# Performance work log

Measured on AMD Instinct MI355X. Metric: run time of the kernel, lower is better.

Reference implementation:

```python
import jax, jax.numpy as jnp
import numpy as np

N_NODES = 50000


def gat_layer(x, src, dst, W, att_s, att_d, b, concat):
    # PyG GATConv (eval mode): h = x W reshaped to [N, H, C]
    H, C = att_s.shape
    h = (x @ W).reshape(-1, H, C)                      # [N, H, C]
    a_s = (h * att_s).sum(-1)                          # [N, H]
    a_d = (h * att_d).sum(-1)                          # [N, H]
    e = jax.nn.leaky_relu(a_s[src] + a_d[dst], 0.2)    # [E, H]
    # scatter-softmax over destination nodes
    m = jax.ops.segment_max(e, dst, num_segments=N_NODES)
    alpha = jnp.exp(e - m[dst])
    denom = jax.ops.segment_sum(alpha, dst, num_segments=N_NODES)
    alpha = alpha / denom[dst]                         # [E, H]
    msg = h[src] * alpha[:, :, None]                   # [E, H, C]
    out = jax.ops.segment_sum(msg, dst, num_segments=N_NODES)  # [N, H, C]
    out = out.reshape(N_NODES, H * C) if concat else out.mean(axis=1)
    return out + b


def setup_inputs() -> dict:
    key = jax.random.key(0)
    ks = jax.random.split(key, 16)
    F_IN, HID, HEADS, NCLS, E = 512, 64, 4, 40, 800000
    x = jax.random.normal(ks[0], (N_NODES, F_IN), dtype=jnp.float32)
    edge_index = jax.random.randint(ks[1], (2, E), 0, N_NODES, dtype=jnp.int32)

    def glorot(k, shape):
        fan = shape[0]
        return jax.random.normal(k, shape, dtype=jnp.float32) / np.sqrt(fan)

    d1 = HID * HEADS  # 256
    return {
        "x": x,
        "edge_index": edge_index,
        "W1": glorot(ks[2], (F_IN, d1)),
        "as1": glorot(ks[3], (HEADS, HID)),
        "ad1": glorot(ks[4], (HEADS, HID)),
        "b1": jnp.zeros((d1,), jnp.float32),
        "W2": glorot(ks[5], (d1, d1)),
        "as2": glorot(ks[6], (HEADS, HID)),
        "ad2": glorot(ks[7], (HEADS, HID)),
        "b2": jnp.zeros((d1,), jnp.float32),
        "W3": glorot(ks[8], (d1, NCLS)),
        "as3": glorot(ks[9], (1, NCLS)),
        "ad3": glorot(ks[10], (1, NCLS)),
        "b3": jnp.zeros((NCLS,), jnp.float32),
    }


def reference(x, edge_index, W1, as1, ad1, b1, W2, as2, ad2, b2, W3, as3, ad3, b3):
    # add self-loops (PyG GATConv default)
    loops = jnp.arange(N_NODES, dtype=edge_index.dtype)
    src = jnp.concatenate([edge_index[0], loops])
    dst = jnp.concatenate([edge_index[1], loops])
    h = jax.nn.elu(gat_layer(x, src, dst, W1, as1, ad1, b1, True))
    h = jax.nn.elu(gat_layer(h, src, dst, W2, as2, ad2, b2, True))
    out = gat_layer(h, src, dst, W3, as3, ad3, b3, False)
    return out
```

## Files before the change

### kernel.cpp

```cpp
#include <hip/hip_runtime.h>
#include <stdint.h>

#define NN 50000
#define NB 196

typedef unsigned short u16;
typedef _Float16 f16;
typedef __attribute__((ext_vector_type(8))) _Float16 half8;
typedef __attribute__((ext_vector_type(4))) _Float16 half4;
typedef __attribute__((ext_vector_type(4))) float f32x4;


__global__ void count_k(const int* __restrict__ dst, int* __restrict__ cnt, int E){
  int i = blockIdx.x * 256 + threadIdx.x;
  int tot = E + NN;
  if (i >= tot) return;
  int d = (i < E) ? dst[i] : (i - E);
  atomicAdd(&cnt[d], 1);
}

__global__ __launch_bounds__(256) void scan_part_k(const int* __restrict__ cnt,
                                                   int* __restrict__ bsum){
  __shared__ int lds[256];
  int tid = threadIdx.x;
  int idx = blockIdx.x * 256 + tid;
  lds[tid] = (idx < NN) ? cnt[idx] : 0;
  __syncthreads();
#pragma unroll
  for (int off = 128; off >= 1; off >>= 1){
    if (tid < off) lds[tid] += lds[tid + off];
    __syncthreads();
  }
  if (tid == 0) bsum[blockIdx.x] = lds[0];
}

__global__ __launch_bounds__(256) void scan_top_k(const int* __restrict__ bsum,
                                                  int* __restrict__ boff,
                                                  int* __restrict__ row_ptr){
  __shared__ int lds[256];
  int tid = threadIdx.x;
  int v = (tid < NB) ? bsum[tid] : 0;
  lds[tid] = v;
  __syncthreads();
#pragma unroll
  for (int off = 1; off < 256; off <<= 1){
    int t = (tid >= off) ? lds[tid - off] : 0;
    __syncthreads();
    lds[tid] += t;
    __syncthreads();
  }
  if (tid < NB) boff[tid] = lds[tid] - v;
  if (tid == 255) row_ptr[NN] = lds[255];
}

__global__ __launch_bounds__(256) void scan_fin_k(const int* __restrict__ cnt,
                                                  const int* __restrict__ boff,
                                                  int* __restrict__ row_ptr,
                                                  int* __restrict__ cursor){
  __shared__ int lds[256];
  int tid = threadIdx.x;
  int idx = blockIdx.x * 256 + tid;
  int v = (idx < NN) ? cnt[idx] : 0;
  lds[tid] = v;
  __syncthreads();
#pragma unroll
  for (int off = 1; off < 256; off <<= 1){
    int t = (tid >= off) ? lds[tid - off] : 0;
    __syncthreads();
    lds[tid] += t;
    __syncthreads();
  }
  if (idx < NN){
    int r = boff[blockIdx.x] + lds[tid] - v;
    row_ptr[idx] = r;
    cursor[idx]  = r;
  }
}

__global__ void scatter_k(const int* __restrict__ src, const int* __restrict__ dst,
                          int* __restrict__ cursor, int* __restrict__ csr, int E){
  int i = blockIdx.x * 256 + threadIdx.x;
  int tot = E + NN;
  if (i >= tot) return;
  int s, d;
  if (i < E){ s = src[i]; d = dst[i]; } else { s = i - E; d = i - E; }
  int pos = atomicAdd(&cursor[d], 1);
  csr[pos] = s;
}


__global__ void transpose_k(const float* __restrict__ W, f16* __restrict__ Wt, int K, int N){
  int i = blockIdx.x * 256 + threadIdx.x;
  if (i >= K * N) return;
  int n = i / K, k = i - n * K;
  Wt[i] = (f16)W[k * N + n];
}


template<bool A_FP32>
__global__ __launch_bounds__(256) void gemm_wide_k(const void* __restrict__ Aptr,
                                                   const f16* __restrict__ Bt,
                                                   f16* __restrict__ C,
                                                   int M, int K){
  __shared__ f16 As[64 * 40];
  __shared__ f16 Bs[256 * 40];
  const int tid  = threadIdx.x;
  const int wave = tid >> 6, lane = tid & 63;
  const int quad = lane >> 4, l16 = lane & 15;
  const int m0 = blockIdx.x * 64;
  const int srow = tid >> 2;
  const int scol = (tid & 3) * 8;

  f32x4 acc[16] = {};

  for (int k0 = 0; k0 < K; k0 += 32){
    half8 va = {0,0,0,0,0,0,0,0};
    int gm = m0 + srow;
    if (gm < M){
      if (A_FP32){
        const float* A = (const float*)Aptr;
        const f32x4 f0 = *(const f32x4*)(A + (size_t)gm * K + k0 + scol);
        const f32x4 f1 = *(const f32x4*)(A + (size_t)gm * K + k0 + scol + 4);
        va[0] = (f16)f0.x; va[1] = (f16)f0.y; va[2] = (f16)f0.z; va[3] = (f16)f0.w;
        va[4] = (f16)f1.x; va[5] = (f16)f1.y; va[6] = (f16)f1.z; va[7] = (f16)f1.w;
      } else {
        va = *(const half8*)((const f16*)Aptr + (size_t)gm * K + k0 + scol);
      }
    }
    *(half8*)(&As[srow * 40 + scol]) = va;

#pragma unroll
    for (int rep = 0; rep < 4; rep++){
      int row = srow + 64 * rep;
      half8 vb = *(const half8*)(Bt + (size_t)row * K + k0 + scol);
      *(half8*)(&Bs[row * 40 + scol]) = vb;
    }

    __syncthreads();
    half8 af = *(const half8*)(&As[(wave * 16 + l16) * 40 + quad * 8]);
#pragma unroll
    for (int i = 0; i < 16; i++){
      half8 bf = *(const half8*)(&Bs[(i * 16 + l16) * 40 + quad * 8]);
      acc[i] = __builtin_amdgcn_mfma_f32_16x16x32_f16(af, bf, acc[i], 0, 0, 0);
    }
    __syncthreads();
  }

#pragma unroll
  for (int i = 0; i < 16; i++){
    int n = i * 16 + l16;
#pragma unroll
    for (int r = 0; r < 4; r++){
      int mm = m0 + wave * 16 + quad * 4 + r;
      if (mm < M) C[(size_t)mm * 256 + n] = (f16)acc[i][r];
    }
  }
}


__global__ __launch_bounds__(256) void gemm_k(const f16* __restrict__ A,
                                              const f16* __restrict__ Bt,
                                              f16* __restrict__ C,
                                              int M, int N, int K){
  __shared__ f16 As[64 * 40];
  __shared__ f16 Bs[64 * 40];
  const int tid  = threadIdx.x;
  const int wave = tid >> 6, lane = tid & 63;
  const int quad = lane >> 4, l16 = lane & 15;
  const int m0 = blockIdx.x * 64, n0 = blockIdx.y * 64;
  const int srow = tid >> 2;
  const int scol = (tid & 3) * 8;

  f32x4 acc[4] = {};

  for (int k0 = 0; k0 < K; k0 += 32){
    half8 va = {0,0,0,0,0,0,0,0};
    int gm = m0 + srow;
    if (gm < M) va = *(const half8*)(A + (size_t)gm * K + k0 + scol);
    *(half8*)(&As[srow * 40 + scol]) = va;

    half8 vb = {0,0,0,0,0,0,0,0};
    int gn = n0 + srow;
    if (gn < N) vb = *(const half8*)(Bt + (size_t)gn * K + k0 + scol);
    *(half8*)(&Bs[srow * 40 + scol]) = vb;

    __syncthreads();
    half8 af = *(const half8*)(&As[(wave * 16 + l16) * 40 + quad * 8]);
#pragma unroll
    for (int i = 0; i < 4; i++){
      half8 bf = *(const half8*)(&Bs[(i * 16 + l16) * 40 + quad * 8]);
      acc[i] = __builtin_amdgcn_mfma_f32_16x16x32_f16(af, bf, acc[i], 0, 0, 0);
    }
    __syncthreads();
  }

#pragma unroll
  for (int i = 0; i < 4; i++){
    int n = n0 + i * 16 + l16;
#pragma unroll
    for (int r = 0; r < 4; r++){
      int m = m0 + wave * 16 + quad * 4 + r;
      if (m < M && n < N) C[(size_t)m * N + n] = (f16)acc[i][r];
    }
  }
}


__global__ __launch_bounds__(256) void attn4_k(const f16* __restrict__ h,
                                               const float* __restrict__ atts,
                                               const float* __restrict__ attd,
                                               float* __restrict__ a_s,
                                               float* __restrict__ a_d){
  int w = blockIdx.x * 4 + (threadIdx.x >> 6);
  if (w >= NN) return;
  int lane = threadIdx.x & 63;
  const half4 hv = *(const half4*)(h + (size_t)w * 256 + lane * 4);
  const f32x4 sv = *(const f32x4*)(atts + lane * 4);
  const f32x4 dv = *(const f32x4*)(attd + lane * 4);
  float h0 = (float)hv.x, h1 = (float)hv.y, h2 = (float)hv.z, h3 = (float)hv.w;
  float ps = h0 * sv.x + h1 * sv.y + h2 * sv.z + h3 * sv.w;
  float pd = h0 * dv.x + h1 * dv.y + h2 * dv.z + h3 * dv.w;
#pragma unroll
  for (int off = 8; off >= 1; off >>= 1){
    ps += __shfl_xor(ps, off);
    pd += __shfl_xor(pd, off);
  }
  if ((lane & 15) == 0){
    a_s[w * 4 + (lane >> 4)] = ps;
    a_d[w * 4 + (lane >> 4)] = pd;
  }
}

__global__ __launch_bounds__(256) void attn1_k(const f16* __restrict__ h,
                                               const float* __restrict__ atts,
                                               const float* __restrict__ attd,
                                               float* __restrict__ a_s,
                                               float* __restrict__ a_d){
  int w = blockIdx.x * 4 + (threadIdx.x >> 6);
  if (w >= NN) return;
  int lane = threadIdx.x & 63;
  float ps = 0.f, pd = 0.f;
  if (lane < 40){
    float hv = (float)h[(size_t)w * 40 + lane];
    ps = hv * atts[lane];
    pd = hv * attd[lane];
  }
#pragma unroll
  for (int off = 32; off >= 1; off >>= 1){
    ps += __shfl_xor(ps, off);
    pd += __shfl_xor(pd, off);
  }
  if (lane == 0){ a_s[w] = ps; a_d[w] = pd; }
}


__device__ __forceinline__ float lrelu(float e){ return e > 0.f ? e : 0.2f * e; }

__global__ __launch_bounds__(256) void agg4_k(const f16* __restrict__ h,
                                              const float* __restrict__ a_s,
                                              const float* __restrict__ a_d,
                                              const int* __restrict__ row_ptr,
                                              const int* __restrict__ csr,
                                              const float* __restrict__ bias,
                                              f16* __restrict__ out){
  int w = blockIdx.x * 4 + (threadIdx.x >> 6);
  if (w >= NN) return;
  int lane = threadIdx.x & 63;
  int head = lane >> 4;
  float ad = a_d[w * 4 + head];
  int beg = row_ptr[w], end = row_ptr[w + 1];

  float m = -1e30f, denom = 0.f;
  float acc0 = 0.f, acc1 = 0.f, acc2 = 0.f, acc3 = 0.f;

  int s0 = csr[beg];
  int s1 = csr[(beg + 1 < end) ? beg + 1 : beg];
  float e0 = a_s[s0 * 4 + head];
  float e1 = a_s[s1 * 4 + head];
  half4 h0 = *(const half4*)(h + (size_t)s0 * 256 + lane * 4);
  half4 h1 = *(const half4*)(h + (size_t)s1 * 256 + lane * 4);

  for (int j = beg; j < end; j += 2){
    int t0 = (j + 2 < end) ? j + 2 : j;
    int t1 = (j + 3 < end) ? j + 3 : j;
    int sp0 = csr[t0], sp1 = csr[t1];
    float ep0 = a_s[sp0 * 4 + head];
    float ep1 = a_s[sp1 * 4 + head];
    half4 hp0 = *(const half4*)(h + (size_t)sp0 * 256 + lane * 4);
    half4 hp1 = *(const half4*)(h + (size_t)sp1 * 256 + lane * 4);

    float ee0 = lrelu(e0 + ad);
    float ee1 = (j + 1 < end) ? lrelu(e1 + ad) : -1e30f;
    float mn = fmaxf(m, fmaxf(ee0, ee1));
    float cold = __expf(m - mn);
    float al0 = __expf(ee0 - mn);
    float al1 = __expf(ee1 - mn);
    denom = denom * cold + al0 + al1;
    acc0 = acc0 * cold + al0 * (float)h0.x + al1 * (float)h1.x;
    acc1 = acc1 * cold + al0 * (float)h0.y + al1 * (float)h1.y;
    acc2 = acc2 * cold + al0 * (float)h0.z + al1 * (float)h1.z;
    acc3 = acc3 * cold + al0 * (float)h0.w + al1 * (float)h1.w;
    m = mn;
    e0 = ep0; e1 = ep1; h0 = hp0; h1 = hp1;
  }

  float inv = 1.f / fmaxf(denom, 1e-30f);
  float o0 = acc0 * inv + bias[lane * 4 + 0];
  float o1 = acc1 * inv + bias[lane * 4 + 1];
  float o2 = acc2 * inv + bias[lane * 4 + 2];
  float o3 = acc3 * inv + bias[lane * 4 + 3];
  o0 = o0 > 0.f ? o0 : __expf(o0) - 1.f;
  o1 = o1 > 0.f ? o1 : __expf(o1) - 1.f;
  o2 = o2 > 0.f ? o2 : __expf(o2) - 1.f;
  o3 = o3 > 0.f ? o3 : __expf(o3) - 1.f;
  half4 r; r.x = (f16)o0; r.y = (f16)o1; r.z = (f16)o2; r.w = (f16)o3;
  *(half4*)(out + (size_t)w * 256 + lane * 4) = r;
}

__global__ __launch_bounds__(256) void agg1_k(const f16* __restrict__ h,
                                              const float* __restrict__ a_s,
                                              const float* __restrict__ a_d,
                                              const int* __restrict__ row_ptr,
                                              const int* __restrict__ csr,
                                              const float* __restrict__ bias,
                                              float* __restrict__ out){
  int w = blockIdx.x * 4 + (threadIdx.x >> 6);
  if (w >= NN) return;
  int lane = threadIdx.x & 63;
  int cl = (lane < 40) ? lane : 0;
  float ad = a_d[w];
  int beg = row_ptr[w], end = row_ptr[w + 1];

  float m = -1e30f, denom = 0.f, acc = 0.f;

  int s0 = csr[beg];
  int s1 = csr[(beg + 1 < end) ? beg + 1 : beg];
  float e0 = a_s[s0];
  float e1 = a_s[s1];
  float h0 = (float)h[(size_t)s0 * 40 + cl];
  float h1 = (float)h[(size_t)s1 * 40 + cl];

  for (int j = beg; j < end; j += 2){
    int t0 = (j + 2 < end) ? j + 2 : j;
    int t1 = (j + 3 < end) ? j + 3 : j;
    int sp0 = csr[t0], sp1 = csr[t1];
    float ep0 = a_s[sp0];
    float ep1 = a_s[sp1];
    float hp0 = (float)h[(size_t)sp0 * 40 + cl];
    float hp1 = (float)h[(size_t)sp1 * 40 + cl];

    float ee0 = lrelu(e0 + ad);
    float ee1 = (j + 1 < end) ? lrelu(e1 + ad) : -1e30f;
    float mn = fmaxf(m, fmaxf(ee0, ee1));
    float cold = __expf(m - mn);
    float al0 = __expf(ee0 - mn);
    float al1 = __expf(ee1 - mn);
    denom = denom * cold + al0 + al1;
    acc = acc * cold + al0 * h0 + al1 * h1;
    m = mn;
    e0 = ep0; e1 = ep1; h0 = hp0; h1 = hp1;
  }

  if (lane < 40){
    float o = acc / fmaxf(denom, 1e-30f) + bias[lane];
    out[(size_t)w * 40 + lane] = o;
  }
}


extern "C" void kernel_launch(void* const* d_in, const int* in_sizes, int n_in,
                              void* d_out, int out_size, void* d_ws, size_t ws_size,
                              hipStream_t stream){
  const float* x   = (const float*)d_in[0];
  const int*   ei  = (const int*)d_in[1];
  const float* W1  = (const float*)d_in[2];
  const float* as1 = (const float*)d_in[3];
  const float* ad1 = (const float*)d_in[4];
  const float* b1  = (const float*)d_in[5];
  const float* W2  = (const float*)d_in[6];
  const float* as2 = (const float*)d_in[7];
  const float* ad2 = (const float*)d_in[8];
  const float* b2  = (const float*)d_in[9];
  const float* W3  = (const float*)d_in[10];
  const float* as3 = (const float*)d_in[11];
  const float* ad3 = (const float*)d_in[12];
  const float* b3  = (const float*)d_in[13];

  const int E = in_sizes[1] / 2;
  const int ETOT = E + NN;
  const int* src_arr = ei;
  const int* dst_arr = ei + E;

  char* ws = (char*)d_ws;
  size_t off = 0;
  auto alloc = [&](size_t bytes) -> void* {
    void* p = ws + off; off += (bytes + 255) & ~(size_t)255; return p;
  };
  int*   cnt     = (int*)  alloc((size_t)NN * 4);
  int*   row_ptr = (int*)  alloc((size_t)(NN + 1) * 4);
  int*   cursor  = (int*)  alloc((size_t)NN * 4);
  int*   csr     = (int*)  alloc((size_t)ETOT * 4);
  int*   bsum    = (int*)  alloc((size_t)256 * 4);
  int*   boff    = (int*)  alloc((size_t)256 * 4);
  f16*   W1t     = (f16*)  alloc((size_t)512 * 256 * 2);
  f16*   W2t     = (f16*)  alloc((size_t)256 * 256 * 2);
  f16*   W3t     = (f16*)  alloc((size_t)256 * 40 * 2);
  float* a_s     = (float*)alloc((size_t)NN * 4 * 4);
  float* a_d     = (float*)alloc((size_t)NN * 4 * 4);
  f16*   hbuf    = (f16*)  alloc((size_t)NN * 256 * 2);
  f16*   xbuf    = (f16*)  alloc((size_t)NN * 256 * 2);
  (void)ws_size; (void)n_in; (void)out_size;

  hipMemsetAsync(cnt, 0, (size_t)NN * 4, stream);
  int egrid = (ETOT + 255) / 256;
  count_k    <<<egrid, 256, 0, stream>>>(dst_arr, cnt, E);
  scan_part_k<<<NB, 256, 0, stream>>>(cnt, bsum);
  scan_top_k <<<1, 256, 0, stream>>>(bsum, boff, row_ptr);
  scan_fin_k <<<NB, 256, 0, stream>>>(cnt, boff, row_ptr, cursor);
  scatter_k  <<<egrid, 256, 0, stream>>>(src_arr, dst_arr, cursor, csr, E);

  transpose_k<<<(512 * 256 + 255) / 256, 256, 0, stream>>>(W1, W1t, 512, 256);
  transpose_k<<<(256 * 256 + 255) / 256, 256, 0, stream>>>(W2, W2t, 256, 256);
  transpose_k<<<(256 * 40  + 255) / 256, 256, 0, stream>>>(W3, W3t, 256, 40);

  dim3 blk(256);
  dim3 gW((NN + 63) / 64);
  dim3 gC((NN + 63) / 64, 1);
  int nodeblocks = (NN + 3) / 4;

  gemm_wide_k<true> <<<gW, blk, 0, stream>>>(x, W1t, hbuf, NN, 512);
  attn4_k<<<nodeblocks, blk, 0, stream>>>(hbuf, as1, ad1, a_s, a_d);
  agg4_k <<<nodeblocks, blk, 0, stream>>>(hbuf, a_s, a_d, row_ptr, csr, b1, xbuf);

  gemm_wide_k<false><<<gW, blk, 0, stream>>>(xbuf, W2t, hbuf, NN, 256);
  attn4_k<<<nodeblocks, blk, 0, stream>>>(hbuf, as2, ad2, a_s, a_d);
  agg4_k <<<nodeblocks, blk, 0, stream>>>(hbuf, a_s, a_d, row_ptr, csr, b2, xbuf);

  gemm_k<<<gC, blk, 0, stream>>>(xbuf, W3t, hbuf, NN, 40, 256);
  attn1_k<<<nodeblocks, blk, 0, stream>>>(hbuf, as3, ad3, a_s, a_d);
  agg1_k <<<nodeblocks, blk, 0, stream>>>(hbuf, a_s, a_d, row_ptr, csr, b3, (float*)d_out);
}
```

Baseline: 592.0 us.

## Retile wide GEMM to 128x128 blocks with 2x2 wave grid and swizzled LDS

Replaces the 64x256 row-strip GEMM with a 128x128 tile kernel where each of four waves computes a 64x64 sub-tile via 4x4 MFMA accumulators, and the grid now spans two column blocks. LDS is stored in an MFMA-fragment-friendly layout so each lane reads contiguous half8 fragments without padding. This raises per-wave register reuse of A and B fragments and cuts LDS reads per MFMA. In exchange it uses more accumulator registers, which may lower occupancy, and the A tile is loaded twice across the two column blocks.

```diff
diff --git a/kernel.cpp b/kernel.cpp
--- a/kernel.cpp
+++ b/kernel.cpp
@@ -98,61 +98,74 @@
 
 
 template<bool A_FP32>
-__global__ __launch_bounds__(256) void gemm_wide_k(const void* __restrict__ Aptr,
+__global__ __launch_bounds__(256) void gemm_tile_k(const void* __restrict__ Aptr,
                                                    const f16* __restrict__ Bt,
                                                    f16* __restrict__ C,
-                                                   int M, int K){
-  __shared__ f16 As[64 * 40];
-  __shared__ f16 Bs[256 * 40];
+                                                   int M, int N, int K){
+  __shared__ f16 As[128 * 32];
+  __shared__ f16 Bs[128 * 32];
   const int tid  = threadIdx.x;
   const int wave = tid >> 6, lane = tid & 63;
   const int quad = lane >> 4, l16 = lane & 15;
-  const int m0 = blockIdx.x * 64;
+  const int wm = wave >> 1, wn = wave & 1;
+  const int m0 = blockIdx.x * 128, n0 = blockIdx.y * 128;
   const int srow = tid >> 2;
-  const int scol = (tid & 3) * 8;
-
-  f32x4 acc[16] = {};
+  const int sc   = tid & 3;
+
+  f32x4 acc[4][4] = {};
 
   for (int k0 = 0; k0 < K; k0 += 32){
-    half8 va = {0,0,0,0,0,0,0,0};
-    int gm = m0 + srow;
-    if (gm < M){
-      if (A_FP32){
-        const float* A = (const float*)Aptr;
-        const f32x4 f0 = *(const f32x4*)(A + (size_t)gm * K + k0 + scol);
-        const f32x4 f1 = *(const f32x4*)(A + (size_t)gm * K + k0 + scol + 4);
-        va[0] = (f16)f0.x; va[1] = (f16)f0.y; va[2] = (f16)f0.z; va[3] = (f16)f0.w;
-        va[4] = (f16)f1.x; va[5] = (f16)f1.y; va[6] = (f16)f1.z; va[7] = (f16)f1.w;
-      } else {
-        va = *(const half8*)((const f16*)Aptr + (size_t)gm * K + k0 + scol);
+#pragma unroll
+    for (int rep = 0; rep < 2; rep++){
+      int row = rep * 64 + srow;
+      int gm = m0 + row;
+      half8 va = {0,0,0,0,0,0,0,0};
+      if (gm < M){
+        if (A_FP32){
+          const float* A = (const float*)Aptr + (size_t)gm * K + k0 + sc * 8;
+          const f32x4 f0 = *(const f32x4*)(A);
+          const f32x4 f1 = *(const f32x4*)(A + 4);
+          va[0] = (f16)f0.x; va[1] = (f16)f0.y; va[2] = (f16)f0.z; va[3] = (f16)f0.w;
+          va[4] = (f16)f1.x; va[5] = (f16)f1.y; va[6] = (f16)f1.z; va[7] = (f16)f1.w;
+        } else {
+          va = *(const half8*)((const f16*)Aptr + (size_t)gm * K + k0 + sc * 8);
+        }
       }
+      *(half8*)(&As[(((row >> 4) * 64) + sc * 16 + (row & 15)) * 8]) = va;
     }
-    *(half8*)(&As[srow * 40 + scol]) = va;
-
-#pragma unroll
-    for (int rep = 0; rep < 4; rep++){
-      int row = srow + 64 * rep;
-      half8 vb = *(const half8*)(Bt + (size_t)row * K + k0 + scol);
-      *(half8*)(&Bs[row * 40 + scol]) = vb;
+#pragma unroll
+    for (int rep = 0; rep < 2; rep++){
+      int row = rep * 64 + srow;
+      half8 vb = *(const half8*)(Bt + (size_t)(n0 + row) * K + k0 + sc * 8);
+      *(half8*)(&Bs[(((row >> 4) * 64) + sc * 16 + (row & 15)) * 8]) = vb;
     }
 
     __syncthreads();
-    half8 af = *(const half8*)(&As[(wave * 16 + l16) * 40 + quad * 8]);
-#pragma unroll
-    for (int i = 0; i < 16; i++){
-      half8 bf = *(const half8*)(&Bs[(i * 16 + l16) * 40 + quad * 8]);
-      acc[i] = __builtin_amdgcn_mfma_f32_16x16x32_f16(af, bf, acc[i], 0, 0, 0);
-    }
-    __syncthreads();
-  }
-
-#pragma unroll
-  for (int i = 0; i < 16; i++){
-    int n = i * 16 + l16;
-#pragma unroll
-    for (int r = 0; r < 4; r++){
-      int mm = m0 + wave * 16 + quad * 4 + r;
-      if (mm < M) C[(size_t)mm * 256 + n] = (f16)acc[i][r];
+    half8 af[4], bf[4];
+#pragma unroll
+    for (int i = 0; i < 4; i++)
+      af[i] = *(const half8*)(&As[((wm * 4 + i) * 64 + lane) * 8]);
+#pragma unroll
+    for (int j = 0; j < 4; j++)
+      bf[j] = *(const half8*)(&Bs[((wn * 4 + j) * 64 + lane) * 8]);
+#pragma unroll
+    for (int i = 0; i < 4; i++)
+#pragma unroll
+      for (int j = 0; j < 4; j++)
+        acc[i][j] = __builtin_amdgcn_mfma_f32_16x16x32_f16(af[i], bf[j], acc[i][j], 0, 0, 0);
+    __syncthreads();
+  }
+
+#pragma unroll
+  for (int i = 0; i < 4; i++){
+#pragma unroll
+    for (int j = 0; j < 4; j++){
+      int n = n0 + (wn * 4 + j) * 16 + l16;
+#pragma unroll
+      for (int r = 0; r < 4; r++){
+        int mm = m0 + (wm * 4 + i) * 16 + quad * 4 + r;
+        if (mm < M) C[(size_t)mm * N + n] = (f16)acc[i][j][r];
+      }
     }
   }
 }
@@ -424,15 +437,15 @@
   transpose_k<<<(256 * 40  + 255) / 256, 256, 0, stream>>>(W3, W3t, 256, 40);
 
   dim3 blk(256);
-  dim3 gW((NN + 63) / 64);
+  dim3 gT((NN + 127) / 128, 2);
   dim3 gC((NN + 63) / 64, 1);
   int nodeblocks = (NN + 3) / 4;
 
-  gemm_wide_k<true> <<<gW, blk, 0, stream>>>(x, W1t, hbuf, NN, 512);
+  gemm_tile_k<true> <<<gT, blk, 0, stream>>>(x, W1t, hbuf, NN, 256, 512);
   attn4_k<<<nodeblocks, blk, 0, stream>>>(hbuf, as1, ad1, a_s, a_d);
   agg4_k <<<nodeblocks, blk, 0, stream>>>(hbuf, a_s, a_d, row_ptr, csr, b1, xbuf);
 
-  gemm_wide_k<false><<<gW, blk, 0, stream>>>(xbuf, W2t, hbuf, NN, 256);
+  gemm_tile_k<false><<<gT, blk, 0, stream>>>(xbuf, W2t, hbuf, NN, 256, 256);
   attn4_k<<<nodeblocks, blk, 0, stream>>>(hbuf, as2, ad2, a_s, a_d);
   agg4_k <<<nodeblocks, blk, 0, stream>>>(hbuf, a_s, a_d, row_ptr, csr, b2, xbuf);
 
```

Result: faster. 562.6 us (-5.0%).
